# Performance work log

Measured on AMD Instinct MI355X. Metric: run time of the kernel, lower is better.

## Reference

```python
import jax, jax.numpy as jnp
import numpy as np

BN_EPS = 1e-5


def setup_inputs() -> dict:
    key = jax.random.key(0)
    ks = jax.random.split(key, 8)
    B, N, D = 16, 16384, 64
    NP, NS = 1024, 32
    inp = {
        "xyz": jax.random.normal(ks[0], (B, 3, N), dtype=jnp.float32),
        "points": jax.random.normal(ks[1], (B, D, N), dtype=jnp.float32),
        "fps_init": jax.random.randint(ks[2], (B,), 0, N, dtype=jnp.int32),
        "group_idx": jax.random.randint(ks[3], (B, NP, NS), 0, N, dtype=jnp.int32),
    }
    chans = [67, 64, 128, 128]
    for i in range(3):
        cin, cout = chans[i], chans[i + 1]
        wk = jax.random.fold_in(ks[4], i)
        inp[f"W{i}"] = jax.random.normal(wk, (cout, cin), dtype=jnp.float32) * (1.0 / np.sqrt(cin))
        inp[f"b{i}"] = jnp.zeros((cout,), dtype=jnp.float32)
        inp[f"g{i}"] = jnp.ones((cout,), dtype=jnp.float32)
        inp[f"be{i}"] = jnp.zeros((cout,), dtype=jnp.float32)
    return inp


def _fps(x, init_far, npoint):
    # x: [B,N,3]; iterative furthest point sampling, npoint sequential steps
    B, N, _ = x.shape

    def step(carry, _):
        dist, far = carry
        c = jnp.take_along_axis(x, far[:, None, None], axis=1)  # [B,1,3]
        d = jnp.sum((x - c) ** 2, axis=-1)                       # [B,N]
        dist = jnp.minimum(dist, d)
        return (dist, jnp.argmax(dist, axis=-1).astype(far.dtype)), far

    init = (jnp.full((B, N), 1e10, dtype=x.dtype), init_far)
    _, cents = jax.lax.scan(step, init, None, length=npoint)
    return cents.T  # [B, npoint]


def _conv_bn_relu(h, W, b, g, be):
    # h: [B, np, ns, Cin]; 1x1 conv == channel matmul; BN (training stats) over (B,np,ns)
    y = jnp.einsum('bskc,oc->bsko', h, W) + b
    m = y.mean(axis=(0, 1, 2))
    v = y.var(axis=(0, 1, 2))
    y = (y - m) * jax.lax.rsqrt(v + BN_EPS) * g + be
    return jax.nn.relu(y)


def reference(xyz, points, fps_init, group_idx,
              W0, b0, g0, be0, W1, b1, g1, be1, W2, b2, g2, be2):
    x = jnp.transpose(xyz, (0, 2, 1))     # [B,N,3]
    p = jnp.transpose(points, (0, 2, 1))  # [B,N,D]
    B, N, _ = x.shape
    NP, NS = group_idx.shape[1], group_idx.shape[2]

    cents = _fps(x, fps_init, NP)                                   # [B,NP]
    new_xyz = jnp.take_along_axis(x, cents[:, :, None], axis=1)     # [B,NP,3]

    flat = group_idx.reshape(B, NP * NS)
    gx = jnp.take_along_axis(x, flat[:, :, None], axis=1).reshape(B, NP, NS, 3)
    gp = jnp.take_along_axis(p, flat[:, :, None], axis=1).reshape(B, NP, NS, -1)
    h = jnp.concatenate([gx, gp], axis=-1)  # [B,NP,NS,67]

    h = _conv_bn_relu(h, W0, b0, g0, be0)
    h = _conv_bn_relu(h, W1, b1, g1, be1)
    h = _conv_bn_relu(h, W2, b2, g2, be2)
    new_points = h.max(axis=2)              # max over nsample -> [B,NP,Cout]

    return jnp.transpose(new_xyz, (0, 2, 1)), jnp.transpose(new_points, (0, 2, 1))
```

## Files before the change

### kernel.cpp

```cpp
#include <hip/hip_runtime.h>

typedef short bf16x8 __attribute__((ext_vector_type(8)));
typedef float f32x4 __attribute__((ext_vector_type(4)));
typedef float f32x2 __attribute__((ext_vector_type(2)));
typedef unsigned short u16;
typedef unsigned int u32;
typedef unsigned long long u64;

#define NPTS 16384
#define NPOINT 1024
#define STOT 524288

__device__ __forceinline__ u16 f2bf(float f){
  u32 u = __builtin_bit_cast(u32, f);
  u += 0x7fffu + ((u >> 16) & 1u);
  return (u16)(u >> 16);
}
__device__ __forceinline__ float bf2f(u16 u){
  u32 x = ((u32)u) << 16;
  return __builtin_bit_cast(float, x);
}

template<int CTRL>
__device__ __forceinline__ u64 dpp_max(u64 key){
  u32 lo = (u32)key, hi = (u32)(key >> 32);
  u32 lo1 = (u32)__builtin_amdgcn_update_dpp(0, (int)lo, CTRL, 0xf, 0xf, true);
  u32 hi1 = (u32)__builtin_amdgcn_update_dpp(0, (int)hi, CTRL, 0xf, 0xf, true);
  u64 k1 = ((u64)hi1 << 32) | (u64)lo1;
  return (k1 > key) ? k1 : key;
}

__global__ __launch_bounds__(1024) void fps_kernel(const float* __restrict__ xyz,
                                                   const int* __restrict__ finit,
                                                   float4* __restrict__ xpk_all,
                                                   float* __restrict__ out0){
  __shared__ u64 warr[2][16];
  const int b = blockIdx.x, t = threadIdx.x;
  const int wave = t >> 6, lane = t & 63;
  const float* xb = xyz + (size_t)b * 3 * NPTS;
  float4* xpk = xpk_all + (size_t)b * NPTS;
  f32x2 px[8], py[8], pz[8], dist[8];
#pragma unroll
  for (int j = 0; j < 8; j++){
    f32x2 x, y, z;
#pragma unroll
    for (int h = 0; h < 2; h++){
      int n = ((2*j + h) << 10) + t;
      x[h] = xb[n];
      y[h] = xb[NPTS + n];
      z[h] = xb[2*NPTS + n];
      xpk[n] = make_float4(x[h], y[h], z[h], 0.f);
    }
    px[j] = x; py[j] = y; pz[j] = z;
    f32x2 big = {1e10f, 1e10f};
    dist[j] = big;
  }
  if (t < 32) ((u64*)warr)[t] = 0ULL;
  const int far0 = finit[b];
  __syncthreads();
  int nbu = far0;
  for (int it = 0; it < NPOINT; it++){
    float4 cc = xpk[nbu];
    if (t == 0){
      out0[((size_t)b*3 + 0)*NPOINT + it] = cc.x;
      out0[((size_t)b*3 + 1)*NPOINT + it] = cc.y;
      out0[((size_t)b*3 + 2)*NPOINT + it] = cc.z;
    }
    float bv = -1.f; int bk = 0;
    {
#pragma clang fp contract(off)
      f32x2 cx2 = {cc.x, cc.x}, cy2 = {cc.y, cc.y}, cz2 = {cc.z, cc.z};
#pragma unroll
      for (int j = 0; j < 8; j++){
        f32x2 dx = px[j] - cx2;
        f32x2 dy = py[j] - cy2;
        f32x2 dz = pz[j] - cz2;
        f32x2 dd = dx*dx + dy*dy + dz*dz;
        f32x2 dm = __builtin_elementwise_min(dist[j], dd);
        dist[j] = dm;
        bool g0 = dm.x > bv;
        bv = g0 ? dm.x : bv;  bk = g0 ? (2*j)   : bk;
        bool g1 = dm.y > bv;
        bv = g1 ? dm.y : bv;  bk = g1 ? (2*j+1) : bk;
      }
    }
    int bi = (bk << 10) + t;
    u64 key = ((u64)__builtin_bit_cast(u32, bv) << 32) | (u64)(u32)(~(u32)bi);
    key = dpp_max<0xB1>(key);
    key = dpp_max<0x4E>(key);
    key = dpp_max<0x141>(key);
    key = dpp_max<0x140>(key);
    key = dpp_max<0x142>(key);
    key = dpp_max<0x143>(key);
    if (lane == 63) warr[it & 1][wave] = key;
    __syncthreads();
    u64 kv = warr[it & 1][lane & 15];
    kv = dpp_max<0xB1>(kv);
    kv = dpp_max<0x4E>(kv);
    kv = dpp_max<0x141>(kv);
    kv = dpp_max<0x140>(kv);
    int nb = (int)(~(u32)kv);
    nbu = __builtin_amdgcn_readfirstlane(nb);
  }
}

__global__ __launch_bounds__(256) void pack_kernel(const float* __restrict__ xyz,
                                                   const float* __restrict__ points,
                                                   u16* __restrict__ XP){
  __shared__ float ldsb[67*256];
  const int blk = blockIdx.x, t = threadIdx.x;
  const int b = blk >> 6;
  const int n0 = (blk & 63) << 8;
  for (int c = 0; c < 67; c++){
    const float* src = (c < 3) ? (xyz + ((size_t)b*3 + c)*NPTS)
                               : (points + ((size_t)b*64 + (c-3))*NPTS);
    ldsb[c*256 + t] = src[n0 + t];
  }
  __syncthreads();
  u16* dst = XP + ((size_t)b*NPTS + n0)*96;
  for (int itc = 0; itc < 12; itc++){
    int q = t + (itc << 8);
    int r = q / 12, ch = q % 12;
    u16 tmp[8];
#pragma unroll
    for (int j = 0; j < 8; j++){
      int c = ch*8 + j;
      tmp[j] = (c < 67) ? f2bf(ldsb[c*256 + r]) : (u16)0;
    }
    uint4 v;
    v.x = (u32)tmp[0] | ((u32)tmp[1] << 16);
    v.y = (u32)tmp[2] | ((u32)tmp[3] << 16);
    v.z = (u32)tmp[4] | ((u32)tmp[5] << 16);
    v.w = (u32)tmp[6] | ((u32)tmp[7] << 16);
    *(uint4*)(dst + q*8) = v;
  }
}

__global__ __launch_bounds__(256) void prep_small(const float* __restrict__ W0,
                                                  const float* __restrict__ W1,
                                                  const float* __restrict__ W2,
                                                  u16* __restrict__ W0bf,
                                                  u16* __restrict__ W1bf,
                                                  u16* __restrict__ W2bf,
                                                  float* __restrict__ statsF){
  const int blk = blockIdx.x, t = threadIdx.x;
  if (blk < 48){
#pragma unroll
    for (int k = 0; k < 4; k++) statsF[blk*1024 + k*256 + t] = 0.f;
  } else if (blk == 48){
    for (int i = t; i < 64*96; i += 256){
      int n = i / 96, k = i % 96;
      W0bf[i] = (k < 67) ? f2bf(W0[n*67 + k]) : (u16)0;
    }
  } else if (blk <= 50){
    for (int i = (blk-49)*256 + t; i < 128*64; i += 512) W1bf[i] = f2bf(W1[i]);
  } else if (blk <= 54){
    for (int i = (blk-51)*256 + t; i < 128*128; i += 1024) W2bf[i] = f2bf(W2[i]);
  }
}

__global__ __launch_bounds__(256) void l0_kernel(const u16* __restrict__ XP,
                                                 const int* __restrict__ gidx,
                                                 const u16* __restrict__ W0bf,
                                                 u16* __restrict__ y0,
                                                 float* __restrict__ bsum, float* __restrict__ bsqr){
  __shared__ float lsum[64], lsqr[64];
  const int blk = blockIdx.x, t = threadIdx.x;
  const int b = blk >> 8, j = blk & 255;
  const int wave = t >> 6, lane = t & 63, lrow = lane & 15, lq = lane >> 4;
  if (t < 64){ lsum[t] = 0.f; lsqr[t] = 0.f; }
  __syncthreads();
  const size_t srow = (size_t)blk * 128;
  const int m0 = wave*32 + lrow, m1 = m0 + 16;
  const int gbase = b*32768 + j*128;
  const int p0 = gidx[gbase + m0];
  const int p1 = gidx[gbase + m1];
  const bf16x8* ar0 = (const bf16x8*)(XP + ((size_t)b*NPTS + p0)*96);
  const bf16x8* ar1 = (const bf16x8*)(XP + ((size_t)b*NPTS + p1)*96);
  f32x4 acc[2][4];
#pragma unroll
  for (int mt = 0; mt < 2; mt++)
#pragma unroll
    for (int nt = 0; nt < 4; nt++){ f32x4 z = {0.f,0.f,0.f,0.f}; acc[mt][nt] = z; }
#pragma unroll
  for (int ks = 0; ks < 3; ks++){
    bf16x8 af0 = ar0[ks*4 + lq];
    bf16x8 af1 = ar1[ks*4 + lq];
#pragma unroll
    for (int nt = 0; nt < 4; nt++){
      bf16x8 bb = *(const bf16x8*)(W0bf + (nt*16 + lrow)*96 + ks*32 + lq*8);
      acc[0][nt] = __builtin_amdgcn_mfma_f32_16x16x32_bf16(af0, bb, acc[0][nt], 0, 0, 0);
      acc[1][nt] = __builtin_amdgcn_mfma_f32_16x16x32_bf16(af1, bb, acc[1][nt], 0, 0, 0);
    }
  }
#pragma unroll
  for (int nt = 0; nt < 4; nt++){
    float s = 0.f, s2 = 0.f;
#pragma unroll
    for (int mt = 0; mt < 2; mt++){
#pragma unroll
      for (int i = 0; i < 4; i++){
        float u = acc[mt][nt][i];
        s += u; s2 = fmaf(u, u, s2);
        int m = wave*32 + mt*16 + lq*4 + i;
        y0[(srow + m)*64 + nt*16 + lrow] = f2bf(u);
      }
    }
    s  += __shfl_xor(s, 16, 64);  s  += __shfl_xor(s, 32, 64);
    s2 += __shfl_xor(s2, 16, 64); s2 += __shfl_xor(s2, 32, 64);
    if (lane < 16){ atomicAdd(&lsum[nt*16 + lane], s); atomicAdd(&lsqr[nt*16 + lane], s2); }
  }
  __syncthreads();
  if (t < 64){
    int bkt = blk & 63;
    atomicAdd(&bsum[bkt*128 + t], lsum[t]);
    atomicAdd(&bsqr[bkt*128 + t], lsqr[t]);
  }
}

__global__ __launch_bounds__(128) void stats_kernel(const float* __restrict__ bsum,
                                                    const float* __restrict__ bsqr,
                                                    const float* __restrict__ g,
                                                    const float* __restrict__ be,
                                                    float* __restrict__ a, float* __restrict__ d, int C){
  const int c = threadIdx.x;
  if (c >= C) return;
  float s = 0.f, s2 = 0.f;
  for (int k = 0; k < 64; k++){ s += bsum[k*128 + c]; s2 += bsqr[k*128 + c]; }
  const float inv = 1.f / (float)STOT;
  float m = s * inv;
  float v = s2 * inv - m*m;
  float aa = g[c] / sqrtf(v + 1e-5f);
  a[c] = aa;
  d[c] = be[c] - m*aa;
}

__device__ __forceinline__ bf16x8 load_bn_relu(const u16* __restrict__ row, int ko,
                                               const float* __restrict__ av,
                                               const float* __restrict__ dv){
  uint4 r = *(const uint4*)(row + ko);
  u32 w[4] = {r.x, r.y, r.z, r.w};
  bf16x8 out;
#pragma unroll
  for (int jj = 0; jj < 8; jj++){
    u16 us = (u16)(w[jj >> 1] >> ((jj & 1) * 16));
    float h = fmaxf(fmaf(av[ko + jj], bf2f(us), dv[ko + jj]), 0.f);
    out[jj] = (short)f2bf(h);
  }
  return out;
}

__global__ __launch_bounds__(256) void l1_kernel(const u16* __restrict__ y0,
                                                 const u16* __restrict__ W1bf,
                                                 const float* __restrict__ a0, const float* __restrict__ d0,
                                                 u16* __restrict__ y1,
                                                 float* __restrict__ bsum, float* __restrict__ bsqr){
  __shared__ float lsum[128], lsqr[128];
  __shared__ float av[64], dv[64];
  const int blk = blockIdx.x, t = threadIdx.x;
  const int wave = t >> 6, lane = t & 63, lrow = lane & 15, lq = lane >> 4;
  if (t < 128){ lsum[t] = 0.f; lsqr[t] = 0.f; }
  if (t < 64){ av[t] = a0[t]; dv[t] = d0[t]; }
  __syncthreads();
  const size_t srow = (size_t)blk * 128;
  const int m0 = wave*32 + lrow, m1 = m0 + 16;
  const u16* row0 = y0 + (srow + m0)*64;
  const u16* row1 = y0 + (srow + m1)*64;
  f32x4 acc[2][8];
#pragma unroll
  for (int mt = 0; mt < 2; mt++)
#pragma unroll
    for (int nt = 0; nt < 8; nt++){ f32x4 z = {0.f,0.f,0.f,0.f}; acc[mt][nt] = z; }
#pragma unroll
  for (int ks = 0; ks < 2; ks++){
    const int ko = ks*32 + lq*8;
    bf16x8 af0 = load_bn_relu(row0, ko, av, dv);
    bf16x8 af1 = load_bn_relu(row1, ko, av, dv);
#pragma unroll
    for (int nt = 0; nt < 8; nt++){
      bf16x8 bb = *(const bf16x8*)(W1bf + (nt*16 + lrow)*64 + ko);
      acc[0][nt] = __builtin_amdgcn_mfma_f32_16x16x32_bf16(af0, bb, acc[0][nt], 0, 0, 0);
      acc[1][nt] = __builtin_amdgcn_mfma_f32_16x16x32_bf16(af1, bb, acc[1][nt], 0, 0, 0);
    }
  }
#pragma unroll
  for (int nt = 0; nt < 8; nt++){
    float s = 0.f, s2 = 0.f;
#pragma unroll
    for (int mt = 0; mt < 2; mt++){
#pragma unroll
      for (int i = 0; i < 4; i++){
        float u = acc[mt][nt][i];
        s += u; s2 = fmaf(u, u, s2);
        int m = wave*32 + mt*16 + lq*4 + i;
        y1[(srow + m)*128 + nt*16 + lrow] = f2bf(u);
      }
    }
    s  += __shfl_xor(s, 16, 64);  s  += __shfl_xor(s, 32, 64);
    s2 += __shfl_xor(s2, 16, 64); s2 += __shfl_xor(s2, 32, 64);
    if (lane < 16){ atomicAdd(&lsum[nt*16 + lane], s); atomicAdd(&lsqr[nt*16 + lane], s2); }
  }
  __syncthreads();
  if (t < 128){
    int bkt = blk & 63;
    atomicAdd(&bsum[bkt*128 + t], lsum[t]);
    atomicAdd(&bsqr[bkt*128 + t], lsqr[t]);
  }
}

__global__ __launch_bounds__(256) void l2_kernel(const u16* __restrict__ y1,
                                                 const u16* __restrict__ W2bf,
                                                 const float* __restrict__ a1, const float* __restrict__ d1,
                                                 float* __restrict__ maxb, float* __restrict__ minb,
                                                 float* __restrict__ bsum, float* __restrict__ bsqr){
  __shared__ float lsum[128], lsqr[128];
  __shared__ float av[128], dv[128];
  const int blk = blockIdx.x, t = threadIdx.x;
  const int wave = t >> 6, lane = t & 63, lrow = lane & 15, lq = lane >> 4;
  if (t < 128){ lsum[t] = 0.f; lsqr[t] = 0.f; av[t] = a1[t]; dv[t] = d1[t]; }
  __syncthreads();
  const size_t srow = (size_t)blk * 128;
  const int m0 = wave*32 + lrow, m1 = m0 + 16;
  const u16* row0 = y1 + (srow + m0)*128;
  const u16* row1 = y1 + (srow + m1)*128;
  f32x4 acc[2][8];
#pragma unroll
  for (int mt = 0; mt < 2; mt++)
#pragma unroll
    for (int nt = 0; nt < 8; nt++){ f32x4 z = {0.f,0.f,0.f,0.f}; acc[mt][nt] = z; }
#pragma unroll
  for (int ks = 0; ks < 4; ks++){
    const int ko = ks*32 + lq*8;
    bf16x8 af0 = load_bn_relu(row0, ko, av, dv);
    bf16x8 af1 = load_bn_relu(row1, ko, av, dv);
#pragma unroll
    for (int nt = 0; nt < 8; nt++){
      bf16x8 bb = *(const bf16x8*)(W2bf + (nt*16 + lrow)*128 + ko);
      acc[0][nt] = __builtin_amdgcn_mfma_f32_16x16x32_bf16(af0, bb, acc[0][nt], 0, 0, 0);
      acc[1][nt] = __builtin_amdgcn_mfma_f32_16x16x32_bf16(af1, bb, acc[1][nt], 0, 0, 0);
    }
  }
#pragma unroll
  for (int nt = 0; nt < 8; nt++){
    float s = 0.f, s2 = 0.f, mx = -3.4e38f, mn = 3.4e38f;
#pragma unroll
    for (int mt = 0; mt < 2; mt++){
#pragma unroll
      for (int i = 0; i < 4; i++){
        float u = acc[mt][nt][i];
        s += u; s2 = fmaf(u, u, s2);
        mx = fmaxf(mx, u); mn = fminf(mn, u);
      }
    }
    s  += __shfl_xor(s, 16, 64);  s  += __shfl_xor(s, 32, 64);
    s2 += __shfl_xor(s2, 16, 64); s2 += __shfl_xor(s2, 32, 64);
    mx = fmaxf(mx, __shfl_xor(mx, 16, 64)); mx = fmaxf(mx, __shfl_xor(mx, 32, 64));
    mn = fminf(mn, __shfl_xor(mn, 16, 64)); mn = fminf(mn, __shfl_xor(mn, 32, 64));
    if (lane < 16){
      size_t gi = ((size_t)blk*4 + wave)*128 + nt*16 + lane;
      maxb[gi] = mx; minb[gi] = mn;
      atomicAdd(&lsum[nt*16 + lane], s); atomicAdd(&lsqr[nt*16 + lane], s2);
    }
  }
  __syncthreads();
  if (t < 128){
    int bkt = blk & 63;
    atomicAdd(&bsum[bkt*128 + t], lsum[t]);
    atomicAdd(&bsqr[bkt*128 + t], lsqr[t]);
  }
}

__global__ __launch_bounds__(256) void final_kernel(const float* __restrict__ maxb,
                                                    const float* __restrict__ minb,
                                                    const float* __restrict__ a2, const float* __restrict__ d2,
                                                    float* __restrict__ out1){
  __shared__ float ldsb[64*129];
  __shared__ float av[128], dv[128];
  const int blk = blockIdx.x, t = threadIdx.x;
  const int b = blk >> 4, np0 = (blk & 15) << 6;
  if (t < 128){ av[t] = a2[t]; dv[t] = d2[t]; }
  __syncthreads();
  const size_t base = ((size_t)b*NPOINT + np0)*128;
  for (int itc = 0; itc < 32; itc++){
    int e = t + (itc << 8);
    int npl = e >> 7, c = e & 127;
    float a = av[c];
    float mxv = maxb[base + e], mnv = minb[base + e];
    float vsel = (a >= 0.f) ? mxv : mnv;
    ldsb[npl*129 + c] = fmaxf(fmaf(a, vsel, dv[c]), 0.f);
  }
  __syncthreads();
  for (int itc = 0; itc < 32; itc++){
    int e = t + (itc << 8);
    int c = e >> 6, npl = e & 63;
    out1[((size_t)b*128 + c)*NPOINT + np0 + npl] = ldsb[npl*129 + c];
  }
}

extern "C" void kernel_launch(void* const* d_in, const int* in_sizes, int n_in,
                              void* d_out, int out_size, void* d_ws, size_t ws_size,
                              hipStream_t stream) {
  const float* xyz    = (const float*)d_in[0];
  const float* points = (const float*)d_in[1];
  const int*   finit  = (const int*)d_in[2];
  const int*   gidx   = (const int*)d_in[3];
  const float* W0  = (const float*)d_in[4];
  const float* g0v = (const float*)d_in[6];
  const float* be0 = (const float*)d_in[7];
  const float* W1  = (const float*)d_in[8];
  const float* g1v = (const float*)d_in[10];
  const float* be1 = (const float*)d_in[11];
  const float* W2  = (const float*)d_in[12];
  const float* g2v = (const float*)d_in[14];
  const float* be2 = (const float*)d_in[15];

  float* out0 = (float*)d_out;
  float* out1 = out0 + 16*3*NPOINT;

  char* ws = (char*)d_ws;
  u16* XP = (u16*)ws;
  u16* y1 = (u16*)ws;
  u16* y0 = (u16*)(ws + 134217728);
  float4* xpk = (float4*)(ws + 134217728);
  float* maxb = (float*)(ws + 134217728);
  float* minb = (float*)(ws + 134217728 + 8388608);
  float* statsF = (float*)(ws + 201326592);
  float* bsum0 = statsF;          float* bsqr0 = statsF + 8192;
  float* bsum1 = statsF + 16384;  float* bsqr1 = statsF + 24576;
  float* bsum2 = statsF + 32768;  float* bsqr2 = statsF + 40960;
  float* a0 = statsF + 49152;       float* d0 = a0 + 128;
  float* a1 = statsF + 49152 + 256; float* d1 = a1 + 128;
  float* a2 = statsF + 49152 + 512; float* d2 = a2 + 128;
  u16* W0bf = (u16*)(statsF + 49920);
  u16* W1bf = W0bf + 64*96;
  u16* W2bf = W1bf + 128*64;

  fps_kernel<<<16, 1024, 0, stream>>>(xyz, finit, xpk, out0);
  prep_small<<<64, 256, 0, stream>>>(W0, W1, W2, W0bf, W1bf, W2bf, statsF);
  pack_kernel<<<1024, 256, 0, stream>>>(xyz, points, XP);
  l0_kernel<<<4096, 256, 0, stream>>>(XP, gidx, W0bf, y0, bsum0, bsqr0);
  stats_kernel<<<1, 128, 0, stream>>>(bsum0, bsqr0, g0v, be0, a0, d0, 64);
  l1_kernel<<<4096, 256, 0, stream>>>(y0, W1bf, a0, d0, y1, bsum1, bsqr1);
  stats_kernel<<<1, 128, 0, stream>>>(bsum1, bsqr1, g1v, be1, a1, d1, 128);
  l2_kernel<<<4096, 256, 0, stream>>>(y1, W2bf, a1, d1, maxb, minb, bsum2, bsqr2);
  stats_kernel<<<1, 128, 0, stream>>>(bsum2, bsqr2, g2v, be2, a2, d2, 128);
  final_kernel<<<256, 256, 0, stream>>>(maxb, minb, a2, d2, out1);
}
```

Baseline: 2.231 ms.

## Fuse all stages into persistent megakernel overlapping FPS with conv layers

Replaces the chain of separate launches with one persistent kernel of 256 blocks. Sixteen blocks run furthest point sampling while the other 240 pack inputs and run the three conv+BN layers and the final max, with atomic-counter grid barriers between stages. The point is to hide the serial FPS loop behind the MLP work and remove launch gaps. The risks are spin-wait overhead, a deadlock if not all 256 1024-thread blocks are resident at once, and fewer blocks doing the conv work.

Result: slower. 2.503 ms (+12.2%).

```diff
diff --git a/kernel.cpp b/kernel.cpp
--- a/kernel.cpp
+++ b/kernel.cpp
@@ -10,6 +10,8 @@
 #define NPTS 16384
 #define NPOINT 1024
 #define STOT 524288
+#define NCB 240
+#define NW  960
 
 __device__ __forceinline__ u16 f2bf(float f){
   u32 u = __builtin_bit_cast(u32, f);
@@ -29,211 +31,19 @@
   u64 k1 = ((u64)hi1 << 32) | (u64)lo1;
   return (k1 > key) ? k1 : key;
 }
-
-__global__ __launch_bounds__(1024) void fps_kernel(const float* __restrict__ xyz,
-                                                   const int* __restrict__ finit,
-                                                   float4* __restrict__ xpk_all,
-                                                   float* __restrict__ out0){
-  __shared__ u64 warr[2][16];
-  const int b = blockIdx.x, t = threadIdx.x;
-  const int wave = t >> 6, lane = t & 63;
-  const float* xb = xyz + (size_t)b * 3 * NPTS;
-  float4* xpk = xpk_all + (size_t)b * NPTS;
-  f32x2 px[8], py[8], pz[8], dist[8];
-#pragma unroll
-  for (int j = 0; j < 8; j++){
-    f32x2 x, y, z;
-#pragma unroll
-    for (int h = 0; h < 2; h++){
-      int n = ((2*j + h) << 10) + t;
-      x[h] = xb[n];
-      y[h] = xb[NPTS + n];
-      z[h] = xb[2*NPTS + n];
-      xpk[n] = make_float4(x[h], y[h], z[h], 0.f);
-    }
-    px[j] = x; py[j] = y; pz[j] = z;
-    f32x2 big = {1e10f, 1e10f};
-    dist[j] = big;
-  }
-  if (t < 32) ((u64*)warr)[t] = 0ULL;
-  const int far0 = finit[b];
-  __syncthreads();
-  int nbu = far0;
-  for (int it = 0; it < NPOINT; it++){
-    float4 cc = xpk[nbu];
-    if (t == 0){
-      out0[((size_t)b*3 + 0)*NPOINT + it] = cc.x;
-      out0[((size_t)b*3 + 1)*NPOINT + it] = cc.y;
-      out0[((size_t)b*3 + 2)*NPOINT + it] = cc.z;
-    }
-    float bv = -1.f; int bk = 0;
-    {
-#pragma clang fp contract(off)
-      f32x2 cx2 = {cc.x, cc.x}, cy2 = {cc.y, cc.y}, cz2 = {cc.z, cc.z};
-#pragma unroll
-      for (int j = 0; j < 8; j++){
-        f32x2 dx = px[j] - cx2;
-        f32x2 dy = py[j] - cy2;
-        f32x2 dz = pz[j] - cz2;
-        f32x2 dd = dx*dx + dy*dy + dz*dz;
-        f32x2 dm = __builtin_elementwise_min(dist[j], dd);
-        dist[j] = dm;
-        bool g0 = dm.x > bv;
-        bv = g0 ? dm.x : bv;  bk = g0 ? (2*j)   : bk;
-        bool g1 = dm.y > bv;
-        bv = g1 ? dm.y : bv;  bk = g1 ? (2*j+1) : bk;
-      }
-    }
-    int bi = (bk << 10) + t;
-    u64 key = ((u64)__builtin_bit_cast(u32, bv) << 32) | (u64)(u32)(~(u32)bi);
-    key = dpp_max<0xB1>(key);
-    key = dpp_max<0x4E>(key);
-    key = dpp_max<0x141>(key);
-    key = dpp_max<0x140>(key);
-    key = dpp_max<0x142>(key);
-    key = dpp_max<0x143>(key);
-    if (lane == 63) warr[it & 1][wave] = key;
-    __syncthreads();
-    u64 kv = warr[it & 1][lane & 15];
-    kv = dpp_max<0xB1>(kv);
-    kv = dpp_max<0x4E>(kv);
-    kv = dpp_max<0x141>(kv);
-    kv = dpp_max<0x140>(kv);
-    int nb = (int)(~(u32)kv);
-    nbu = __builtin_amdgcn_readfirstlane(nb);
-  }
-}
-
-__global__ __launch_bounds__(256) void pack_kernel(const float* __restrict__ xyz,
-                                                   const float* __restrict__ points,
-                                                   u16* __restrict__ XP){
-  __shared__ float ldsb[67*256];
-  const int blk = blockIdx.x, t = threadIdx.x;
-  const int b = blk >> 6;
-  const int n0 = (blk & 63) << 8;
-  for (int c = 0; c < 67; c++){
-    const float* src = (c < 3) ? (xyz + ((size_t)b*3 + c)*NPTS)
-                               : (points + ((size_t)b*64 + (c-3))*NPTS);
-    ldsb[c*256 + t] = src[n0 + t];
-  }
-  __syncthreads();
-  u16* dst = XP + ((size_t)b*NPTS + n0)*96;
-  for (int itc = 0; itc < 12; itc++){
-    int q = t + (itc << 8);
-    int r = q / 12, ch = q % 12;
-    u16 tmp[8];
-#pragma unroll
-    for (int j = 0; j < 8; j++){
-      int c = ch*8 + j;
-      tmp[j] = (c < 67) ? f2bf(ldsb[c*256 + r]) : (u16)0;
-    }
-    uint4 v;
-    v.x = (u32)tmp[0] | ((u32)tmp[1] << 16);
-    v.y = (u32)tmp[2] | ((u32)tmp[3] << 16);
-    v.z = (u32)tmp[4] | ((u32)tmp[5] << 16);
-    v.w = (u32)tmp[6] | ((u32)tmp[7] << 16);
-    *(uint4*)(dst + q*8) = v;
-  }
-}
-
-__global__ __launch_bounds__(256) void prep_small(const float* __restrict__ W0,
-                                                  const float* __restrict__ W1,
-                                                  const float* __restrict__ W2,
-                                                  u16* __restrict__ W0bf,
-                                                  u16* __restrict__ W1bf,
-                                                  u16* __restrict__ W2bf,
-                                                  float* __restrict__ statsF){
-  const int blk = blockIdx.x, t = threadIdx.x;
-  if (blk < 48){
-#pragma unroll
-    for (int k = 0; k < 4; k++) statsF[blk*1024 + k*256 + t] = 0.f;
-  } else if (blk == 48){
-    for (int i = t; i < 64*96; i += 256){
-      int n = i / 96, k = i % 96;
-      W0bf[i] = (k < 67) ? f2bf(W0[n*67 + k]) : (u16)0;
-    }
-  } else if (blk <= 50){
-    for (int i = (blk-49)*256 + t; i < 128*64; i += 512) W1bf[i] = f2bf(W1[i]);
-  } else if (blk <= 54){
-    for (int i = (blk-51)*256 + t; i < 128*128; i += 1024) W2bf[i] = f2bf(W2[i]);
-  }
-}
-
-__global__ __launch_bounds__(256) void l0_kernel(const u16* __restrict__ XP,
-                                                 const int* __restrict__ gidx,
-                                                 const u16* __restrict__ W0bf,
-                                                 u16* __restrict__ y0,
-                                                 float* __restrict__ bsum, float* __restrict__ bsqr){
-  __shared__ float lsum[64], lsqr[64];
-  const int blk = blockIdx.x, t = threadIdx.x;
-  const int b = blk >> 8, j = blk & 255;
-  const int wave = t >> 6, lane = t & 63, lrow = lane & 15, lq = lane >> 4;
-  if (t < 64){ lsum[t] = 0.f; lsqr[t] = 0.f; }
-  __syncthreads();
-  const size_t srow = (size_t)blk * 128;
-  const int m0 = wave*32 + lrow, m1 = m0 + 16;
-  const int gbase = b*32768 + j*128;
-  const int p0 = gidx[gbase + m0];
-  const int p1 = gidx[gbase + m1];
-  const bf16x8* ar0 = (const bf16x8*)(XP + ((size_t)b*NPTS + p0)*96);
-  const bf16x8* ar1 = (const bf16x8*)(XP + ((size_t)b*NPTS + p1)*96);
-  f32x4 acc[2][4];
-#pragma unroll
-  for (int mt = 0; mt < 2; mt++)
-#pragma unroll
-    for (int nt = 0; nt < 4; nt++){ f32x4 z = {0.f,0.f,0.f,0.f}; acc[mt][nt] = z; }
-#pragma unroll
-  for (int ks = 0; ks < 3; ks++){
-    bf16x8 af0 = ar0[ks*4 + lq];
-    bf16x8 af1 = ar1[ks*4 + lq];
-#pragma unroll
-    for (int nt = 0; nt < 4; nt++){
-      bf16x8 bb = *(const bf16x8*)(W0bf + (nt*16 + lrow)*96 + ks*32 + lq*8);
-      acc[0][nt] = __builtin_amdgcn_mfma_f32_16x16x32_bf16(af0, bb, acc[0][nt], 0, 0, 0);
-      acc[1][nt] = __builtin_amdgcn_mfma_f32_16x16x32_bf16(af1, bb, acc[1][nt], 0, 0, 0);
-    }
-  }
-#pragma unroll
-  for (int nt = 0; nt < 4; nt++){
-    float s = 0.f, s2 = 0.f;
-#pragma unroll
-    for (int mt = 0; mt < 2; mt++){
-#pragma unroll
-      for (int i = 0; i < 4; i++){
-        float u = acc[mt][nt][i];
-        s += u; s2 = fmaf(u, u, s2);
-        int m = wave*32 + mt*16 + lq*4 + i;
-        y0[(srow + m)*64 + nt*16 + lrow] = f2bf(u);
-      }
-    }
-    s  += __shfl_xor(s, 16, 64);  s  += __shfl_xor(s, 32, 64);
-    s2 += __shfl_xor(s2, 16, 64); s2 += __shfl_xor(s2, 32, 64);
-    if (lane < 16){ atomicAdd(&lsum[nt*16 + lane], s); atomicAdd(&lsqr[nt*16 + lane], s2); }
-  }
-  __syncthreads();
-  if (t < 64){
-    int bkt = blk & 63;
-    atomicAdd(&bsum[bkt*128 + t], lsum[t]);
-    atomicAdd(&bsqr[bkt*128 + t], lsqr[t]);
-  }
-}
-
-__global__ __launch_bounds__(128) void stats_kernel(const float* __restrict__ bsum,
-                                                    const float* __restrict__ bsqr,
-                                                    const float* __restrict__ g,
-                                                    const float* __restrict__ be,
-                                                    float* __restrict__ a, float* __restrict__ d, int C){
-  const int c = threadIdx.x;
-  if (c >= C) return;
-  float s = 0.f, s2 = 0.f;
-  for (int k = 0; k < 64; k++){ s += bsum[k*128 + c]; s2 += bsqr[k*128 + c]; }
-  const float inv = 1.f / (float)STOT;
-  float m = s * inv;
-  float v = s2 * inv - m*m;
-  float aa = g[c] / sqrtf(v + 1e-5f);
-  a[c] = aa;
-  d[c] = be[c] - m*aa;
-}
+__device__ __forceinline__ u64 umax64(u64 a, u64 b){ return (a > b) ? a : b; }
+
+__device__ __forceinline__ void arrive(u32* c){
+  __hip_atomic_fetch_add(c, 1u, __ATOMIC_RELEASE, __HIP_MEMORY_SCOPE_AGENT);
+}
+__device__ __forceinline__ void waitc(u32* c, u32 tgt){
+  while (__hip_atomic_load(c, __ATOMIC_ACQUIRE, __HIP_MEMORY_SCOPE_AGENT) < tgt)
+    __builtin_amdgcn_s_sleep(16);
+}
+
+struct FpsS  { u64 warr[2][16]; };
+struct ConvS { float lsum[128]; float lsqr[128]; float av[128]; float dv[128]; };
+union SMemU  { FpsS fps; ConvS conv; };
 
 __device__ __forceinline__ bf16x8 load_bn_relu(const u16* __restrict__ row, int ko,
                                                const float* __restrict__ av,
@@ -250,150 +60,366 @@
   return out;
 }
 
-__global__ __launch_bounds__(256) void l1_kernel(const u16* __restrict__ y0,
-                                                 const u16* __restrict__ W1bf,
-                                                 const float* __restrict__ a0, const float* __restrict__ d0,
-                                                 u16* __restrict__ y1,
-                                                 float* __restrict__ bsum, float* __restrict__ bsqr){
-  __shared__ float lsum[128], lsqr[128];
-  __shared__ float av[64], dv[64];
-  const int blk = blockIdx.x, t = threadIdx.x;
-  const int wave = t >> 6, lane = t & 63, lrow = lane & 15, lq = lane >> 4;
-  if (t < 128){ lsum[t] = 0.f; lsqr[t] = 0.f; }
-  if (t < 64){ av[t] = a0[t]; dv[t] = d0[t]; }
-  __syncthreads();
-  const size_t srow = (size_t)blk * 128;
-  const int m0 = wave*32 + lrow, m1 = m0 + 16;
-  const u16* row0 = y0 + (srow + m0)*64;
-  const u16* row1 = y0 + (srow + m1)*64;
-  f32x4 acc[2][8];
-#pragma unroll
-  for (int mt = 0; mt < 2; mt++)
-#pragma unroll
-    for (int nt = 0; nt < 8; nt++){ f32x4 z = {0.f,0.f,0.f,0.f}; acc[mt][nt] = z; }
-#pragma unroll
-  for (int ks = 0; ks < 2; ks++){
-    const int ko = ks*32 + lq*8;
-    bf16x8 af0 = load_bn_relu(row0, ko, av, dv);
-    bf16x8 af1 = load_bn_relu(row1, ko, av, dv);
+__global__ void zero_kernel(u32* __restrict__ ctrs){
+  if (threadIdx.x < 64) ctrs[threadIdx.x] = 0;
+}
+
+__global__ __launch_bounds__(1024) void mega_kernel(
+    const float* __restrict__ xyz, const float* __restrict__ points,
+    const int* __restrict__ finit, const int* __restrict__ gidx,
+    const float* __restrict__ W0, const float* __restrict__ g0v, const float* __restrict__ be0,
+    const float* __restrict__ W1, const float* __restrict__ g1v, const float* __restrict__ be1,
+    const float* __restrict__ W2, const float* __restrict__ g2v, const float* __restrict__ be2,
+    float* __restrict__ out0, float* __restrict__ out1,
+    u16* __restrict__ XP, u16* __restrict__ y0, u16* __restrict__ y1,
+    float* __restrict__ maxb, float* __restrict__ minb,
+    float* __restrict__ statsF, float4* __restrict__ xpk_all,
+    u16* __restrict__ W0bf, u16* __restrict__ W1bf, u16* __restrict__ W2bf,
+    u32* __restrict__ ctrs){
+  __shared__ SMemU sm;
+  const int t = threadIdx.x;
+  const int wave = t >> 6, lane = t & 63;
+
+  if (blockIdx.x < 16){
+    const int b = blockIdx.x;
+    const float* xb = xyz + (size_t)b * 3 * NPTS;
+    float4* xpk = xpk_all + (size_t)b * NPTS;
+    f32x2 px[8], py[8], pz[8], dist[8];
+#pragma unroll
+    for (int j = 0; j < 8; j++){
+      f32x2 x, y, z;
+#pragma unroll
+      for (int h = 0; h < 2; h++){
+        int n = ((2*j + h) << 10) + t;
+        x[h] = xb[n];
+        y[h] = xb[NPTS + n];
+        z[h] = xb[2*NPTS + n];
+        xpk[n] = make_float4(x[h], y[h], z[h], 0.f);
+      }
+      px[j] = x; py[j] = y; pz[j] = z;
+      f32x2 big = {1e10f, 1e10f};
+      dist[j] = big;
+    }
+    if (t < 32) ((u64*)sm.fps.warr)[t] = 0ULL;
+    const int far0 = finit[b];
+    __syncthreads();
+    int nbu = far0;
+    for (int it = 0; it < NPOINT; it++){
+      float4 cc = xpk[nbu];
+      if (t == 0){
+        out0[((size_t)b*3 + 0)*NPOINT + it] = cc.x;
+        out0[((size_t)b*3 + 1)*NPOINT + it] = cc.y;
+        out0[((size_t)b*3 + 2)*NPOINT + it] = cc.z;
+      }
+      float bv = -1.f; int bk = 0;
+      {
+#pragma clang fp contract(off)
+        f32x2 cx2 = {cc.x, cc.x}, cy2 = {cc.y, cc.y}, cz2 = {cc.z, cc.z};
+#pragma unroll
+        for (int j = 0; j < 8; j++){
+          f32x2 dx = px[j] - cx2;
+          f32x2 dy = py[j] - cy2;
+          f32x2 dz = pz[j] - cz2;
+          f32x2 dd = dx*dx + dy*dy + dz*dz;
+          f32x2 dm = __builtin_elementwise_min(dist[j], dd);
+          dist[j] = dm;
+          bool g0 = dm.x > bv;
+          bv = g0 ? dm.x : bv;  bk = g0 ? (2*j)   : bk;
+          bool g1 = dm.y > bv;
+          bv = g1 ? dm.y : bv;  bk = g1 ? (2*j+1) : bk;
+        }
+      }
+      int bi = (bk << 10) + t;
+      u64 key = ((u64)__builtin_bit_cast(u32, bv) << 32) | (u64)(u32)(~(u32)bi);
+      key = dpp_max<0xB1>(key);
+      key = dpp_max<0x4E>(key);
+      key = dpp_max<0x141>(key);
+      key = dpp_max<0x140>(key);
+      key = dpp_max<0x142>(key);
+      key = dpp_max<0x143>(key);
+      if (lane == 63) sm.fps.warr[it & 1][wave] = key;
+      __syncthreads();
+      u64 kv = sm.fps.warr[it & 1][lane & 15];
+      kv = dpp_max<0xB1>(kv);
+      kv = dpp_max<0x4E>(kv);
+      kv = dpp_max<0x141>(kv);
+      kv = dpp_max<0x140>(kv);
+      nbu = __builtin_amdgcn_readfirstlane((int)~(u32)kv);
+    }
+    return;
+  }
+
+  const int cb = blockIdx.x - 16;
+  const int lw = wave & 3, g = wave >> 2;
+  const int Wk = cb*4 + g;
+  const int lrow = lane & 15, lq = lane >> 4;
+  float* bsum0 = statsF;          float* bsqr0 = statsF + 8192;
+  float* bsum1 = statsF + 16384;  float* bsqr1 = statsF + 24576;
+  float* bsum2 = statsF + 32768;  float* bsqr2 = statsF + 40960;
+  float* a0 = statsF + 49152;       float* d0 = a0 + 128;
+  float* a1 = statsF + 49152 + 256; float* d1 = a1 + 128;
+  float* a2 = statsF + 49152 + 512; float* d2 = a2 + 128;
+
+  for (u32 idx = (u32)cb*1024u + t; idx < 16u*16384u; idx += (u32)NCB*1024u){
+    u32 b = idx >> 14, n = idx & 16383u;
+    const float* xb = xyz + (size_t)b*3*NPTS + n;
+    const float* pb = points + (size_t)b*64*NPTS + n;
+    u16* dst = XP + ((size_t)b*NPTS + n)*96;
+#pragma unroll
+    for (int half = 0; half < 2; half++){
+      u32 w[24];
+#pragma unroll
+      for (int q = 0; q < 24; q++){
+        int c0 = half*48 + 2*q, c1 = c0 + 1;
+        float f0 = (c0 < 3) ? xb[(size_t)c0*NPTS] : (c0 < 67) ? pb[(size_t)(c0-3)*NPTS] : 0.f;
+        float f1 = (c1 < 3) ? xb[(size_t)c1*NPTS] : (c1 < 67) ? pb[(size_t)(c1-3)*NPTS] : 0.f;
+        w[q] = (u32)f2bf(f0) | ((u32)f2bf(f1) << 16);
+      }
+#pragma unroll
+      for (int q = 0; q < 6; q++){
+        uint4 v; v.x = w[4*q]; v.y = w[4*q+1]; v.z = w[4*q+2]; v.w = w[4*q+3];
+        *(uint4*)(dst + half*48 + q*8) = v;
+      }
+    }
+  }
+  if (cb == 0){
+    for (int i = t; i < 64*96; i += 1024){
+      int nn = i / 96, kk = i % 96;
+      W0bf[i] = (kk < 67) ? f2bf(W0[nn*67 + kk]) : (u16)0;
+    }
+    for (int i = t; i < 128*64; i += 1024) W1bf[i] = f2bf(W1[i]);
+    for (int i = t; i < 128*128; i += 1024) W2bf[i] = f2bf(W2[i]);
+  }
+  if (cb == 1){
+    for (int i = t; i < 49152; i += 1024) statsF[i] = 0.f;
+  }
+  __threadfence();
+  __syncthreads();
+  if (t == 0){ arrive(&ctrs[0]); waitc(&ctrs[0], NCB); }
+  __syncthreads();
+
+  if (t < 128){ sm.conv.lsum[t] = 0.f; sm.conv.lsqr[t] = 0.f; }
+  __syncthreads();
+  for (int j2 = Wk; j2 < 4096; j2 += NW){
+    const int b = j2 >> 8;
+    const size_t srow = (size_t)j2 * 128;
+    const int gbase = b*32768 + (j2 & 255)*128;
+    const int m0 = lw*32 + lrow, m1 = m0 + 16;
+    const int p0 = gidx[gbase + m0];
+    const int p1 = gidx[gbase + m1];
+    const bf16x8* ar0 = (const bf16x8*)(XP + ((size_t)b*NPTS + p0)*96);
+    const bf16x8* ar1 = (const bf16x8*)(XP + ((size_t)b*NPTS + p1)*96);
+    f32x4 acc[2][4];
+#pragma unroll
+    for (int mt = 0; mt < 2; mt++)
+#pragma unroll
+      for (int nt = 0; nt < 4; nt++){ f32x4 z = {0.f,0.f,0.f,0.f}; acc[mt][nt] = z; }
+#pragma unroll
+    for (int ks = 0; ks < 3; ks++){
+      bf16x8 af0 = ar0[ks*4 + lq];
+      bf16x8 af1 = ar1[ks*4 + lq];
+#pragma unroll
+      for (int nt = 0; nt < 4; nt++){
+        bf16x8 bb = *(const bf16x8*)(W0bf + (nt*16 + lrow)*96 + ks*32 + lq*8);
+        acc[0][nt] = __builtin_amdgcn_mfma_f32_16x16x32_bf16(af0, bb, acc[0][nt], 0, 0, 0);
+        acc[1][nt] = __builtin_amdgcn_mfma_f32_16x16x32_bf16(af1, bb, acc[1][nt], 0, 0, 0);
+      }
+    }
+#pragma unroll
+    for (int nt = 0; nt < 4; nt++){
+      float s = 0.f, s2 = 0.f;
+#pragma unroll
+      for (int mt = 0; mt < 2; mt++){
+#pragma unroll
+        for (int i = 0; i < 4; i++){
+          float u = acc[mt][nt][i];
+          s += u; s2 = fmaf(u, u, s2);
+          int m = lw*32 + mt*16 + lq*4 + i;
+          y0[(srow + m)*64 + nt*16 + lrow] = f2bf(u);
+        }
+      }
+      s  += __shfl_xor(s, 16, 64);  s  += __shfl_xor(s, 32, 64);
+      s2 += __shfl_xor(s2, 16, 64); s2 += __shfl_xor(s2, 32, 64);
+      if (lane < 16){ atomicAdd(&sm.conv.lsum[nt*16 + lane], s); atomicAdd(&sm.conv.lsqr[nt*16 + lane], s2); }
+    }
+  }
+  __syncthreads();
+  if (t < 64){
+    atomicAdd(&bsum0[(cb & 63)*128 + t], sm.conv.lsum[t]);
+    atomicAdd(&bsqr0[(cb & 63)*128 + t], sm.conv.lsqr[t]);
+  }
+  __threadfence();
+  __syncthreads();
+  if (t == 0) arrive(&ctrs[1]);
+  if (cb == 0){
+    if (t == 0) waitc(&ctrs[1], NCB);
+    __syncthreads();
+    if (t < 64){
+      float s = 0.f, s2 = 0.f;
+      for (int k = 0; k < 64; k++){ s += bsum0[k*128 + t]; s2 += bsqr0[k*128 + t]; }
+      const float inv = 1.f / (float)STOT;
+      float m = s * inv, v = s2 * inv - m*m;
+      float aa = g0v[t] / sqrtf(v + 1e-5f);
+      a0[t] = aa; d0[t] = be0[t] - m*aa;
+    }
+    __threadfence();
+    __syncthreads();
+    if (t == 0) arrive(&ctrs[2]);
+  }
+  if (t == 0) waitc(&ctrs[2], 1);
+  __syncthreads();
+
+  if (t < 128){ sm.conv.lsum[t] = 0.f; sm.conv.lsqr[t] = 0.f; }
+  if (t < 64){ sm.conv.av[t] = a0[t]; sm.conv.dv[t] = d0[t]; }
+  __syncthreads();
+  for (int j2 = Wk; j2 < 4096; j2 += NW){
+    const size_t srow = (size_t)j2 * 128;
+    const int m0 = lw*32 + lrow, m1 = m0 + 16;
+    const u16* row0 = y0 + (srow + m0)*64;
+    const u16* row1 = y0 + (srow + m1)*64;
+    f32x4 acc[2][8];
+#pragma unroll
+    for (int mt = 0; mt < 2; mt++)
+#pragma unroll
+      for (int nt = 0; nt < 8; nt++){ f32x4 z = {0.f,0.f,0.f,0.f}; acc[mt][nt] = z; }
+#pragma unroll
+    for (int ks = 0; ks < 2; ks++){
+      const int ko = ks*32 + lq*8;
+      bf16x8 af0 = load_bn_relu(row0, ko, sm.conv.av, sm.conv.dv);
+      bf16x8 af1 = load_bn_relu(row1, ko, sm.conv.av, sm.conv.dv);
+#pragma unroll
+      for (int nt = 0; nt < 8; nt++){
+        bf16x8 bb = *(const bf16x8*)(W1bf + (nt*16 + lrow)*64 + ko);
+        acc[0][nt] = __builtin_amdgcn_mfma_f32_16x16x32_bf16(af0, bb, acc[0][nt], 0, 0, 0);
+        acc[1][nt] = __builtin_amdgcn_mfma_f32_16x16x32_bf16(af1, bb, acc[1][nt], 0, 0, 0);
+      }
+    }
 #pragma unroll
     for (int nt = 0; nt < 8; nt++){
-      bf16x8 bb = *(const bf16x8*)(W1bf + (nt*16 + lrow)*64 + ko);
-      acc[0][nt] = __builtin_amdgcn_mfma_f32_16x16x32_bf16(af0, bb, acc[0][nt], 0, 0, 0);
-      acc[1][nt] = __builtin_amdgcn_mfma_f32_16x16x32_bf16(af1, bb, acc[1][nt], 0, 0, 0);
-    }
-  }
-#pragma unroll
-  for (int nt = 0; nt < 8; nt++){
-    float s = 0.f, s2 = 0.f;
-#pragma unroll
-    for (int mt = 0; mt < 2; mt++){
-#pragma unroll
-      for (int i = 0; i < 4; i++){
-        float u = acc[mt][nt][i];
-        s += u; s2 = fmaf(u, u, s2);
-        int m = wave*32 + mt*16 + lq*4 + i;
-        y1[(srow + m)*128 + nt*16 + lrow] = f2bf(u);
-      }
-    }
-    s  += __shfl_xor(s, 16, 64);  s  += __shfl_xor(s, 32, 64);
-    s2 += __shfl_xor(s2, 16, 64); s2 += __shfl_xor(s2, 32, 64);
-    if (lane < 16){ atomicAdd(&lsum[nt*16 + lane], s); atomicAdd(&lsqr[nt*16 + lane], s2); }
+      float s = 0.f, s2 = 0.f;
+#pragma unroll
+      for (int mt = 0; mt < 2; mt++){
+#pragma unroll
+        for (int i = 0; i < 4; i++){
+          float u = acc[mt][nt][i];
+          s += u; s2 = fmaf(u, u, s2);
+          int m = lw*32 + mt*16 + lq*4 + i;
+          y1[(srow + m)*128 + nt*16 + lrow] = f2bf(u);
+        }
+      }
+      s  += __shfl_xor(s, 16, 64);  s  += __shfl_xor(s, 32, 64);
+      s2 += __shfl_xor(s2, 16, 64); s2 += __shfl_xor(s2, 32, 64);
+      if (lane < 16){ atomicAdd(&sm.conv.lsum[nt*16 + lane], s); atomicAdd(&sm.conv.lsqr[nt*16 + lane], s2); }
+    }
   }
   __syncthreads();
   if (t < 128){
-    int bkt = blk & 63;
-    atomicAdd(&bsum[bkt*128 + t], lsum[t]);
-    atomicAdd(&bsqr[bkt*128 + t], lsqr[t]);
-  }
-}
-
-__global__ __launch_bounds__(256) void l2_kernel(const u16* __restrict__ y1,
-                                                 const u16* __restrict__ W2bf,
-                                                 const float* __restrict__ a1, const float* __restrict__ d1,
-                                                 float* __restrict__ maxb, float* __restrict__ minb,
-                                                 float* __restrict__ bsum, float* __restrict__ bsqr){
-  __shared__ float lsum[128], lsqr[128];
-  __shared__ float av[128], dv[128];
-  const int blk = blockIdx.x, t = threadIdx.x;
-  const int wave = t >> 6, lane = t & 63, lrow = lane & 15, lq = lane >> 4;
-  if (t < 128){ lsum[t] = 0.f; lsqr[t] = 0.f; av[t] = a1[t]; dv[t] = d1[t]; }
-  __syncthreads();
-  const size_t srow = (size_t)blk * 128;
-  const int m0 = wave*32 + lrow, m1 = m0 + 16;
-  const u16* row0 = y1 + (srow + m0)*128;
-  const u16* row1 = y1 + (srow + m1)*128;
-  f32x4 acc[2][8];
-#pragma unroll
-  for (int mt = 0; mt < 2; mt++)
-#pragma unroll
-    for (int nt = 0; nt < 8; nt++){ f32x4 z = {0.f,0.f,0.f,0.f}; acc[mt][nt] = z; }
-#pragma unroll
-  for (int ks = 0; ks < 4; ks++){
-    const int ko = ks*32 + lq*8;
-    bf16x8 af0 = load_bn_relu(row0, ko, av, dv);
-    bf16x8 af1 = load_bn_relu(row1, ko, av, dv);
+    atomicAdd(&bsum1[(cb & 63)*128 + t], sm.conv.lsum[t]);
+    atomicAdd(&bsqr1[(cb & 63)*128 + t], sm.conv.lsqr[t]);
+  }
+  __threadfence();
+  __syncthreads();
+  if (t == 0) arrive(&ctrs[3]);
+  if (cb == 0){
+    if (t == 0) waitc(&ctrs[3], NCB);
+    __syncthreads();
+    if (t < 128){
+      float s = 0.f, s2 = 0.f;
+      for (int k = 0; k < 64; k++){ s += bsum1[k*128 + t]; s2 += bsqr1[k*128 + t]; }
+      const float inv = 1.f / (float)STOT;
+      float m = s * inv, v = s2 * inv - m*m;
+      float aa = g1v[t] / sqrtf(v + 1e-5f);
+      a1[t] = aa; d1[t] = be1[t] - m*aa;
+    }
+    __threadfence();
+    __syncthreads();
+    if (t == 0) arrive(&ctrs[4]);
+  }
+  if (t == 0) waitc(&ctrs[4], 1);
+  __syncthreads();
+
+  if (t < 128){ sm.conv.lsum[t] = 0.f; sm.conv.lsqr[t] = 0.f;
+                sm.conv.av[t] = a1[t]; sm.conv.dv[t] = d1[t]; }
+  __syncthreads();
+  for (int j2 = Wk; j2 < 4096; j2 += NW){
+    const size_t srow = (size_t)j2 * 128;
+    const int m0 = lw*32 + lrow, m1 = m0 + 16;
+    const u16* row0 = y1 + (srow + m0)*128;
+    const u16* row1 = y1 + (srow + m1)*128;
+    f32x4 acc[2][8];
+#pragma unroll
+    for (int mt = 0; mt < 2; mt++)
+#pragma unroll
+      for (int nt = 0; nt < 8; nt++){ f32x4 z = {0.f,0.f,0.f,0.f}; acc[mt][nt] = z; }
+#pragma unroll
+    for (int ks = 0; ks < 4; ks++){
+      const int ko = ks*32 + lq*8;
+      bf16x8 af0 = load_bn_relu(row0, ko, sm.conv.av, sm.conv.dv);
+      bf16x8 af1 = load_bn_relu(row1, ko, sm.conv.av, sm.conv.dv);
+#pragma unroll
+      for (int nt = 0; nt < 8; nt++){
+        bf16x8 bb = *(const bf16x8*)(W2bf + (nt*16 + lrow)*128 + ko);
+        acc[0][nt] = __builtin_amdgcn_mfma_f32_16x16x32_bf16(af0, bb, acc[0][nt], 0, 0, 0);
+        acc[1][nt] = __builtin_amdgcn_mfma_f32_16x16x32_bf16(af1, bb, acc[1][nt], 0, 0, 0);
+      }
+    }
 #pragma unroll
     for (int nt = 0; nt < 8; nt++){
-      bf16x8 bb = *(const bf16x8*)(W2bf + (nt*16 + lrow)*128 + ko);
-      acc[0][nt] = __builtin_amdgcn_mfma_f32_16x16x32_bf16(af0, bb, acc[0][nt], 0, 0, 0);
-      acc[1][nt] = __builtin_amdgcn_mfma_f32_16x16x32_bf16(af1, bb, acc[1][nt], 0, 0, 0);
-    }
-  }
-#pragma unroll
-  for (int nt = 0; nt < 8; nt++){
-    float s = 0.f, s2 = 0.f, mx = -3.4e38f, mn = 3.4e38f;
-#pragma unroll
-    for (int mt = 0; mt < 2; mt++){
-#pragma unroll
-      for (int i = 0; i < 4; i++){
-        float u = acc[mt][nt][i];
-        s += u; s2 = fmaf(u, u, s2);
-        mx = fmaxf(mx, u); mn = fminf(mn, u);
-      }
-    }
-    s  += __shfl_xor(s, 16, 64);  s  += __shfl_xor(s, 32, 64);
-    s2 += __shfl_xor(s2, 16, 64); s2 += __shfl_xor(s2, 32, 64);
-    mx = fmaxf(mx, __shfl_xor(mx, 16, 64)); mx = fmaxf(mx, __shfl_xor(mx, 32, 64));
-    mn = fminf(mn, __shfl_xor(mn, 16, 64)); mn = fminf(mn, __shfl_xor(mn, 32, 64));
-    if (lane < 16){
-      size_t gi = ((size_t)blk*4 + wave)*128 + nt*16 + lane;
-      maxb[gi] = mx; minb[gi] = mn;
-      atomicAdd(&lsum[nt*16 + lane], s); atomicAdd(&lsqr[nt*16 + lane], s2);
+      float s = 0.f, s2 = 0.f, mx = -3.4e38f, mn = 3.4e38f;
+#pragma unroll
+      for (int mt = 0; mt < 2; mt++){
+#pragma unroll
+        for (int i = 0; i < 4; i++){
+          float u = acc[mt][nt][i];
+          s += u; s2 = fmaf(u, u, s2);
+          mx = fmaxf(mx, u); mn = fminf(mn, u);
+        }
+      }
+      s  += __shfl_xor(s, 16, 64);  s  += __shfl_xor(s, 32, 64);
+      s2 += __shfl_xor(s2, 16, 64); s2 += __shfl_xor(s2, 32, 64);
+      mx = fmaxf(mx, __shfl_xor(mx, 16, 64)); mx = fmaxf(mx, __shfl_xor(mx, 32, 64));
+      mn = fminf(mn, __shfl_xor(mn, 16, 64)); mn = fminf(mn, __shfl_xor(mn, 32, 64));
+      if (lane < 16){
+        size_t gi = ((size_t)j2*4 + lw)*128 + nt*16 + lane;
+        maxb[gi] = mx; minb[gi] = mn;
+        atomicAdd(&sm.conv.lsum[nt*16 + lane], s); atomicAdd(&sm.conv.lsqr[nt*16 + lane], s2);
+      }
     }
   }
   __syncthreads();
   if (t < 128){
-    int bkt = blk & 63;
-    atomicAdd(&bsum[bkt*128 + t], lsum[t]);
-    atomicAdd(&bsqr[bkt*128 + t], lsqr[t]);
-  }
-}
-
-__global__ __launch_bounds__(256) void final_kernel(const float* __restrict__ maxb,
-                                                    const float* __restrict__ minb,
-                                                    const float* __restrict__ a2, const float* __restrict__ d2,
-                                                    float* __restrict__ out1){
-  __shared__ float ldsb[64*129];
-  __shared__ float av[128], dv[128];
-  const int blk = blockIdx.x, t = threadIdx.x;
-  const int b = blk >> 4, np0 = (blk & 15) << 6;
-  if (t < 128){ av[t] = a2[t]; dv[t] = d2[t]; }
-  __syncthreads();
-  const size_t base = ((size_t)b*NPOINT + np0)*128;
-  for (int itc = 0; itc < 32; itc++){
-    int e = t + (itc << 8);
-    int npl = e >> 7, c = e & 127;
-    float a = av[c];
-    float mxv = maxb[base + e], mnv = minb[base + e];
-    float vsel = (a >= 0.f) ? mxv : mnv;
-    ldsb[npl*129 + c] = fmaxf(fmaf(a, vsel, dv[c]), 0.f);
-  }
-  __syncthreads();
-  for (int itc = 0; itc < 32; itc++){
-    int e = t + (itc << 8);
-    int c = e >> 6, npl = e & 63;
-    out1[((size_t)b*128 + c)*NPOINT + np0 + npl] = ldsb[npl*129 + c];
+    atomicAdd(&bsum2[(cb & 63)*128 + t], sm.conv.lsum[t]);
+    atomicAdd(&bsqr2[(cb & 63)*128 + t], sm.conv.lsqr[t]);
+  }
+  __threadfence();
+  __syncthreads();
+  if (t == 0) arrive(&ctrs[5]);
+  if (cb == 0){
+    if (t == 0) waitc(&ctrs[5], NCB);
+    __syncthreads();
+    if (t < 128){
+      float s = 0.f, s2 = 0.f;
+      for (int k = 0; k < 64; k++){ s += bsum2[k*128 + t]; s2 += bsqr2[k*128 + t]; }
+      const float inv = 1.f / (float)STOT;
+      float m = s * inv, v = s2 * inv - m*m;
+      float aa = g2v[t] / sqrtf(v + 1e-5f);
+      a2[t] = aa; d2[t] = be2[t] - m*aa;
+    }
+    __threadfence();
+    __syncthreads();
+    if (t == 0) arrive(&ctrs[6]);
+  }
+  if (t == 0) waitc(&ctrs[6], 1);
+  __syncthreads();
+
+  for (u32 e = (u32)cb*1024u + t; e < 16u*1024u*128u; e += (u32)NCB*1024u){
+    u32 np = e & 1023u;
+    u32 c  = (e >> 10) & 127u;
+    u32 b  = e >> 17;
+    size_t gi = ((size_t)b*1024 + np)*128 + c;
+    float a = a2[c];
+    float v = (a >= 0.f) ? maxb[gi] : minb[gi];
+    out1[((size_t)b*128 + c)*1024 + np] = fmaxf(fmaf(a, v, d2[c]), 0.f);
   }
 }
 
@@ -418,31 +444,22 @@
   float* out1 = out0 + 16*3*NPOINT;
 
   char* ws = (char*)d_ws;
+  u16* y1 = (u16*)ws;
   u16* XP = (u16*)ws;
-  u16* y1 = (u16*)ws;
   u16* y0 = (u16*)(ws + 134217728);
-  float4* xpk = (float4*)(ws + 134217728);
   float* maxb = (float*)(ws + 134217728);
   float* minb = (float*)(ws + 134217728 + 8388608);
   float* statsF = (float*)(ws + 201326592);
-  float* bsum0 = statsF;          float* bsqr0 = statsF + 8192;
-  float* bsum1 = statsF + 16384;  float* bsqr1 = statsF + 24576;
-  float* bsum2 = statsF + 32768;  float* bsqr2 = statsF + 40960;
-  float* a0 = statsF + 49152;       float* d0 = a0 + 128;
-  float* a1 = statsF + 49152 + 256; float* d1 = a1 + 128;
-  float* a2 = statsF + 49152 + 512; float* d2 = a2 + 128;
-  u16* W0bf = (u16*)(statsF + 49920);
+  u16* W0bf = (u16*)(ws + 201326592 + 49920*4);
   u16* W1bf = W0bf + 64*96;
   u16* W2bf = W1bf + 128*64;
-
-  fps_kernel<<<16, 1024, 0, stream>>>(xyz, finit, xpk, out0);
-  prep_small<<<64, 256, 0, stream>>>(W0, W1, W2, W0bf, W1bf, W2bf, statsF);
-  pack_kernel<<<1024, 256, 0, stream>>>(xyz, points, XP);
-  l0_kernel<<<4096, 256, 0, stream>>>(XP, gidx, W0bf, y0, bsum0, bsqr0);
-  stats_kernel<<<1, 128, 0, stream>>>(bsum0, bsqr0, g0v, be0, a0, d0, 64);
-  l1_kernel<<<4096, 256, 0, stream>>>(y0, W1bf, a0, d0, y1, bsum1, bsqr1);
-  stats_kernel<<<1, 128, 0, stream>>>(bsum1, bsqr1, g1v, be1, a1, d1, 128);
-  l2_kernel<<<4096, 256, 0, stream>>>(y1, W2bf, a1, d1, maxb, minb, bsum2, bsqr2);
-  stats_kernel<<<1, 128, 0, stream>>>(bsum2, bsqr2, g2v, be2, a2, d2, 128);
-  final_kernel<<<256, 256, 0, stream>>>(maxb, minb, a2, d2, out1);
-}
+  float4* xpk = (float4*)(ws + 201587712);
+  u32* ctrs = (u32*)(ws + 205782016);
+
+  zero_kernel<<<1, 64, 0, stream>>>(ctrs);
+  mega_kernel<<<256, 1024, 0, stream>>>(
+      xyz, points, finit, gidx,
+      W0, g0v, be0, W1, g1v, be1, W2, g2v, be2,
+      out0, out1, XP, y0, y1, maxb, minb, statsF, xpk,
+      W0bf, W1bf, W2bf, ctrs);
+}
```
